# Kernel optimization log

Measured on AMD Instinct MI355X. Metric: run time of the kernel, lower is better.

The kernel has to match this reference:

```python
import jax, jax.numpy as jnp
import numpy as np
from jax import lax

H = 50; W = 50; C = 512; A = 9; P = 3; K = 2048; NC = 20
DIN = C * P * P  # 4608, flattened ROI-pooled feature


def _conv(x, w, b):
    # x [N,H,W,Cin], w [kh,kw,Cin,Cout]
    return lax.conv_general_dilated(x, w, (1, 1), 'SAME',
                                    dimension_numbers=('NHWC', 'HWIO', 'NHWC')) + b


def _roi_align(feat, boxes):
    # feat [H,W,C]; boxes [K,4] = (x1,x2,y1,y2) in feature-map coords -> [K,P,P,C]
    Hf, Wf, _ = feat.shape
    t = (jnp.arange(P, dtype=feat.dtype) + 0.5) / P
    xs = boxes[:, 0:1] + (boxes[:, 1:2] - boxes[:, 0:1]) * t  # [K,P]
    ys = boxes[:, 2:3] + (boxes[:, 3:4] - boxes[:, 2:3]) * t  # [K,P]
    x0f = jnp.floor(xs); y0f = jnp.floor(ys)
    fx = (xs - x0f)[:, None, :, None]  # [K,1,P,1]
    fy = (ys - y0f)[:, :, None, None]  # [K,P,1,1]
    x0 = jnp.clip(x0f.astype(jnp.int32), 0, Wf - 1); x1i = jnp.clip(x0 + 1, 0, Wf - 1)
    y0 = jnp.clip(y0f.astype(jnp.int32), 0, Hf - 1); y1i = jnp.clip(y0 + 1, 0, Hf - 1)

    def g(yi, xi):  # [K,P],[K,P] -> [K,P,P,C]
        return feat[yi[:, :, None], xi[:, None, :]]

    return (g(y0, x0) * (1 - fy) * (1 - fx) + g(y0, x1i) * (1 - fy) * fx
            + g(y1i, x0) * fy * (1 - fx) + g(y1i, x1i) * fy * fx)


def setup_inputs() -> dict:
    key = jax.random.key(0)
    ks = jax.random.split(key, 16)

    def w(k, shape, fan_in):
        return jax.random.normal(k, shape, jnp.float32) / np.float32(np.sqrt(fan_in))

    return {
        'features': jax.random.normal(ks[0], (1, H, W, C), jnp.float32),
        'labels': jax.random.randint(ks[1], (NC,), 0, 2, dtype=jnp.int32),
        'rpn_w': w(ks[2], (2, 2, C, C), 4 * C), 'rpn_b': jnp.zeros((C,), jnp.float32),
        'cls_w': w(ks[3], (1, 1, C, A), C), 'cls_b': jnp.zeros((A,), jnp.float32),
        'reg_w': w(ks[4], (1, 1, C, 4 * A), C), 'reg_b': jnp.zeros((4 * A,), jnp.float32),
        'fc6_w': w(ks[5], (DIN, 9216), DIN), 'fc6_b': jnp.zeros((9216,), jnp.float32),
        'fc7_w': w(ks[6], (9216, 4096), 9216), 'fc7_b': jnp.zeros((4096,), jnp.float32),
        'fc8c_w': w(ks[7], (4096, NC), 4096), 'fc8c_b': jnp.zeros((NC,), jnp.float32),
        'fc8d_w': w(ks[8], (4096, NC), 4096), 'fc8d_b': jnp.zeros((NC,), jnp.float32),
    }


def reference(features, labels, rpn_w, rpn_b, cls_w, cls_b, reg_w, reg_b,
              fc6_w, fc6_b, fc7_w, fc7_b, fc8c_w, fc8c_b, fc8d_w, fc8d_b):
    # RPN head
    x = jax.nn.relu(_conv(features, rpn_w, rpn_b))
    obj = jax.nn.sigmoid(_conv(x, cls_w, cls_b))  # [1,H,W,A] objectness
    reg = _conv(x, reg_w, reg_b)
    # Objectness filtering: fixed-size top-K replaces dynamic threshold filter
    _, idx = lax.top_k(obj.reshape(-1), K)
    raw = reg.reshape(-1, 4)[idx]                 # [K,4]
    s = jax.nn.sigmoid(raw)
    Wd = jnp.float32(W); Hd = jnp.float32(H)
    x1 = s[:, 0] * (Wd - 2.0); x2 = x1 + 1.0 + s[:, 1] * (Wd - 1.0 - x1)
    y1 = s[:, 2] * (Hd - 2.0); y2 = y1 + 1.0 + s[:, 3] * (Hd - 1.0 - y1)
    # original slices feature map with integer coords -> non-differentiable
    boxes = lax.stop_gradient(jnp.stack([x1, x2, y1, y2], axis=1))  # [K,4]
    # Per-ROI pooling (vectorized ROI-align)
    pooled = _roi_align(features[0], boxes).reshape(K, -1)  # [K,DIN]
    # FC trunk + two-stream WSDDN head
    h = jax.nn.relu(pooled @ fc6_w + fc6_b)
    h = jax.nn.relu(h @ fc7_w + fc7_b)
    c = jax.nn.softmax(h @ fc8c_w + fc8c_b, axis=0)  # softmax over regions
    d = jax.nn.softmax(h @ fc8d_w + fc8d_b, axis=1)  # softmax over classes
    scores = c * d                                   # [K,NC]
    output = jnp.clip(jnp.sum(scores, axis=0), 0.0, 1.0)  # [NC]
    return output, scores, boxes
```

## Files before the change

### kernel.cpp

```cpp
#include <hip/hip_runtime.h>
#include <math.h>


#define HN 50
#define WN 50
#define CN 512
#define AN 9
#define KTOP 2048
#define NCL 20
#define NOBJ 22500

typedef unsigned short ushort_t;
typedef __attribute__((ext_vector_type(8))) short short8;
typedef __attribute__((ext_vector_type(4))) float floatx4;

__device__ __forceinline__ ushort_t bf16_rne(float f) {
    unsigned int u = __float_as_uint(f);
    unsigned int r = (u + 0x7FFFu + ((u >> 16) & 1u)) >> 16;
    return (ushort_t)r;
}

__device__ __forceinline__ void gl_lds16(const void* g, void* l) {
    __builtin_amdgcn_global_load_lds(
        (const __attribute__((address_space(1))) unsigned int*)g,
        (__attribute__((address_space(3))) unsigned int*)l, 16, 0, 0);
}

__launch_bounds__(256)
__global__ void conv_chain_kernel(const float* __restrict__ feat,
                                  const float* __restrict__ rpnw,
                                  const float* __restrict__ rpnb,
                                  float* __restrict__ x32)
{
    __shared__ float xs[16 * 512];
    const int tid = threadIdx.x;
    const int hwBase = blockIdx.x * 4;
    const int co0 = tid * 2;

    for (int t = tid; t < 16 * 128; t += 256) {
        int slot = t >> 7, q = t & 127;
        int hwL = slot >> 2, tap = slot & 3;
        int hw = hwBase + hwL;
        int h = hw / WN, w = hw % WN;
        int hy = h + (tap >> 1), wx = w + (tap & 1);
        float4 v = make_float4(0.f, 0.f, 0.f, 0.f);
        if (hy < HN && wx < WN)
            v = *(const float4*)&feat[(size_t)(hy * WN + wx) * CN + q * 4];
        *(float4*)&xs[slot * 512 + q * 4] = v;
    }
    __syncthreads();

    float accx[4][4];
    float accy[4][4];
#pragma unroll
    for (int i = 0; i < 4; i++)
#pragma unroll
        for (int t = 0; t < 4; t++) { accx[i][t] = 0.f; accy[i][t] = 0.f; }

    const float* wbase = rpnw + co0;

    for (int cq = 0; cq < CN; cq += 4) {
        float4 xv[4][4];
#pragma unroll
        for (int i = 0; i < 4; i++)
#pragma unroll
            for (int t = 0; t < 4; t++)
                xv[i][t] = *(const float4*)&xs[(i * 4 + t) * 512 + cq];

#pragma unroll
        for (int cc = 0; cc < 4; cc++) {
            float2 wv[4];
#pragma unroll
            for (int t = 0; t < 4; t++)
                wv[t] = *(const float2*)&wbase[(size_t)(t * CN + cq + cc) * CN];
#pragma unroll
            for (int i = 0; i < 4; i++)
#pragma unroll
                for (int t = 0; t < 4; t++) {
                    float xvv = cc == 0 ? xv[i][t].x
                              : cc == 1 ? xv[i][t].y
                              : cc == 2 ? xv[i][t].z : xv[i][t].w;
                    accx[i][t] = fmaf(xvv, wv[t].x, accx[i][t]);
                    accy[i][t] = fmaf(xvv, wv[t].y, accy[i][t]);
                }
        }
    }

    float b0 = rpnb[co0], b1 = rpnb[co0 + 1];
#pragma unroll
    for (int i = 0; i < 4; i++) {
        float v0 = ((accx[i][0] + accx[i][1]) + accx[i][2]) + accx[i][3];
        float v1 = ((accy[i][0] + accy[i][1]) + accy[i][2]) + accy[i][3];
        v0 = v0 + b0; v1 = v1 + b1;
        v0 = v0 > 0.f ? v0 : 0.f;
        v1 = v1 > 0.f ? v1 : 0.f;
        float2 o = make_float2(v0, v1);
        *(float2*)&x32[(size_t)(hwBase + i) * CN + co0] = o;
    }
}

__launch_bounds__(256)
__global__ void obj_chain_kernel(const float* __restrict__ x32,
                                 const float* __restrict__ clsw,
                                 const float* __restrict__ clsb,
                                 float* __restrict__ key)
{
    int i = blockIdx.x * 256 + threadIdx.x;
    if (i >= NOBJ) return;
    int hw = i / AN, a = i % AN;
    const float* xr = x32 + (size_t)hw * CN;
    float acc = 0.f;
    for (int c = 0; c < CN; c++) acc = fmaf(xr[c], clsw[c * AN + a], acc);
    float l32 = acc + clsb[a];
    float s32 = (float)(1.0 / (1.0 + exp(-(double)l32)));
    key[i] = s32;
}

__launch_bounds__(256)
__global__ void topk_count_kernel(const float* __restrict__ key, int* __restrict__ cnt)
{
    __shared__ float ch[2048];
    int tid = threadIdx.x;
    int j0 = blockIdx.y * 2048;
    for (int t = tid; t < 2048; t += 256) {
        int jg = j0 + t;
        ch[t] = (jg < NOBJ) ? key[jg] : -1.0f;
    }
    int i = blockIdx.x * 256 + tid;
    float vi = (i < NOBJ) ? key[i] : 2.0f;
    __syncthreads();
    int c = 0;
    for (int t = 0; t < 2048; t++) {
        float vj = ch[t];
        int jg = j0 + t;
        c += (vj > vi || (vj == vi && jg < i)) ? 1 : 0;
    }
    if (i < NOBJ && c) atomicAdd(&cnt[i], c);
}

__launch_bounds__(256)
__global__ void topk_scatter_kernel(const int* __restrict__ cnt, int* __restrict__ sorted)
{
    int i = blockIdx.x * 256 + threadIdx.x;
    if (i < NOBJ) {
        int r = cnt[i];
        if (r < KTOP) sorted[r] = i;
    }
}

__launch_bounds__(256)
__global__ void boxes_kernel(const int* __restrict__ sorted,
                             const float* __restrict__ x32,
                             const float* __restrict__ regw,
                             const float* __restrict__ regb,
                             double* __restrict__ boxd,
                             float* __restrict__ outBoxes)
{
    int k = blockIdx.x * 256 + threadIdx.x;
    if (k >= KTOP) return;
    int i = sorted[k];
    int hw = i / AN, a = i % AN;
    const float* xr = x32 + (size_t)hw * CN;
    float r0 = 0.f, r1 = 0.f, r2 = 0.f, r3 = 0.f;
    for (int c = 0; c < CN; c++) {
        float xv = xr[c];
        const float* wr = regw + (size_t)c * (4 * AN) + 4 * a;
        r0 = fmaf(xv, wr[0], r0);
        r1 = fmaf(xv, wr[1], r1);
        r2 = fmaf(xv, wr[2], r2);
        r3 = fmaf(xv, wr[3], r3);
    }
    r0 = r0 + regb[4 * a + 0];
    r1 = r1 + regb[4 * a + 1];
    r2 = r2 + regb[4 * a + 2];
    r3 = r3 + regb[4 * a + 3];
    double s0 = 1.0 / (1.0 + exp(-(double)r0));
    double s1 = 1.0 / (1.0 + exp(-(double)r1));
    double s2 = 1.0 / (1.0 + exp(-(double)r2));
    double s3 = 1.0 / (1.0 + exp(-(double)r3));
    double x1 = s0 * (double)(WN - 2);
    double x2 = x1 + 1.0 + s1 * ((double)(WN - 1) - x1);
    double y1 = s2 * (double)(HN - 2);
    double y2 = y1 + 1.0 + s3 * ((double)(HN - 1) - y1);
    boxd[4 * k + 0] = x1; boxd[4 * k + 1] = x2;
    boxd[4 * k + 2] = y1; boxd[4 * k + 3] = y2;
    outBoxes[4 * k + 0] = (float)x1; outBoxes[4 * k + 1] = (float)x2;
    outBoxes[4 * k + 2] = (float)y1; outBoxes[4 * k + 3] = (float)y2;
}

__launch_bounds__(256)
__global__ void roi_kernel(const float* __restrict__ feat,
                           const double* __restrict__ boxd,
                           ushort_t* __restrict__ pooled)
{
    int k = blockIdx.x;
    int tid = threadIdx.x;
    double x1 = boxd[4 * k + 0], x2 = boxd[4 * k + 1];
    double y1 = boxd[4 * k + 2], y2 = boxd[4 * k + 3];
    int ix0[3], ix1[3], iy0[3], iy1[3];
    double fx[3], fy[3];
#pragma unroll
    for (int p = 0; p < 3; p++) {
        double t = ((double)p + 0.5) / 3.0;
        double xsv = x1 + (x2 - x1) * t;
        double x0f = floor(xsv);
        fx[p] = xsv - x0f;
        int xi = (int)x0f;
        xi = xi < 0 ? 0 : (xi > WN - 1 ? WN - 1 : xi);
        ix0[p] = xi;
        ix1[p] = (xi + 1 > WN - 1) ? WN - 1 : xi + 1;
        double ysv = y1 + (y2 - y1) * t;
        double y0f = floor(ysv);
        fy[p] = ysv - y0f;
        int yi = (int)y0f;
        yi = yi < 0 ? 0 : (yi > HN - 1 ? HN - 1 : yi);
        iy0[p] = yi;
        iy1[p] = (yi + 1 > HN - 1) ? HN - 1 : yi + 1;
    }
#pragma unroll
    for (int pp = 0; pp < 9; pp++) {
        int py = pp / 3, px = pp % 3;
        double w00 = (1.0 - fy[py]) * (1.0 - fx[px]);
        double w01 = (1.0 - fy[py]) * fx[px];
        double w10 = fy[py] * (1.0 - fx[px]);
        double w11 = fy[py] * fx[px];
        const float* f00 = feat + (size_t)(iy0[py] * WN + ix0[px]) * CN;
        const float* f01 = feat + (size_t)(iy0[py] * WN + ix1[px]) * CN;
        const float* f10 = feat + (size_t)(iy1[py] * WN + ix0[px]) * CN;
        const float* f11 = feat + (size_t)(iy1[py] * WN + ix1[px]) * CN;
        ushort_t* dst = pooled + ((size_t)k * 9 + pp) * CN;
        for (int c = tid; c < CN; c += 256) {
            double v = w00 * (double)f00[c] + w01 * (double)f01[c]
                     + w10 * (double)f10[c] + w11 * (double)f11[c];
            dst[c] = bf16_rne((float)v);
        }
    }
}

__launch_bounds__(256)
__global__ void transpose_cvt_kernel(const float* __restrict__ W,
                                     ushort_t* __restrict__ Wt,
                                     int K, int N, int n0)
{
    __shared__ float tile[64][65];
    const int tid = threadIdx.x;
    const int k0 = blockIdx.x * 64;
    const int nb = blockIdx.y * 64;
#pragma unroll
    for (int q = 0; q < 4; q++) {
        int r = (tid >> 4) + q * 16;
        int c = (tid & 15) * 4;
        float4 v = *(const float4*)&W[(size_t)(k0 + r) * N + n0 + nb + c];
        tile[r][c + 0] = v.x; tile[r][c + 1] = v.y;
        tile[r][c + 2] = v.z; tile[r][c + 3] = v.w;
    }
    __syncthreads();
#pragma unroll
    for (int q = 0; q < 4; q++) {
        int rn = (tid >> 4) + q * 16;
        int ck = (tid & 15) * 4;
        ushort4 o;
        o.x = bf16_rne(tile[ck + 0][rn]);
        o.y = bf16_rne(tile[ck + 1][rn]);
        o.z = bf16_rne(tile[ck + 2][rn]);
        o.w = bf16_rne(tile[ck + 3][rn]);
        *(ushort4*)&Wt[(size_t)(nb + rn) * K + k0 + ck] = o;
    }
}

__launch_bounds__(256)
__global__ void pack_w8_kernel(const float* __restrict__ cw,
                               const float* __restrict__ dw,
                               ushort_t* __restrict__ Wt8)
{
    int idx = blockIdx.x * 256 + threadIdx.x;
    int n = idx >> 12, k = idx & 4095;
    float v = 0.f;
    if (n < NCL) v = cw[(size_t)k * NCL + n];
    else if (n < 2 * NCL) v = dw[(size_t)k * NCL + (n - NCL)];
    Wt8[(size_t)n * 4096 + k] = bf16_rne(v);
}

__launch_bounds__(128)
__global__ void pack_b8_kernel(const float* __restrict__ cb,
                               const float* __restrict__ db,
                               float* __restrict__ b8)
{
    int n = threadIdx.x;
    float v = 0.f;
    if (n < NCL) v = cb[n];
    else if (n < 2 * NCL) v = db[n - NCL];
    b8[n] = v;
}

template <bool OUT_BF16, bool RELU>
__launch_bounds__(256)
__global__ void gemm_bt_kernel(const ushort_t* __restrict__ A,
                               const ushort_t* __restrict__ Bt,
                               const float* __restrict__ bias,
                               void* __restrict__ Cv,
                               int Nc, int K)
{
    __shared__ ushort_t As[128 * 32];
    __shared__ ushort_t Bs[128 * 32];
    const int tid = threadIdx.x;
    const int w = tid >> 6, l = tid & 63;
    const int mBase = blockIdx.y * 128, nBase = blockIdx.x * 128;
    const int mW = (w >> 1) * 64, nW = (w & 1) * 64;

    floatx4 acc[4][4];
#pragma unroll
    for (int i = 0; i < 4; i++)
#pragma unroll
        for (int j = 0; j < 4; j++) acc[i][j] = (floatx4){0.f, 0.f, 0.f, 0.f};

    const int r0 = tid >> 2;
    const int ce = (tid & 3) * 8;

    for (int kb = 0; kb < K; kb += 32) {
        __syncthreads();
        gl_lds16(&A[(size_t)(mBase + r0) * K + kb + ce], &As[tid * 8]);
        gl_lds16(&A[(size_t)(mBase + r0 + 64) * K + kb + ce], &As[2048 + tid * 8]);
        gl_lds16(&Bt[(size_t)(nBase + r0) * K + kb + ce], &Bs[tid * 8]);
        gl_lds16(&Bt[(size_t)(nBase + r0 + 64) * K + kb + ce], &Bs[2048 + tid * 8]);
        __syncthreads();

        short8 aF[4], bF[4];
#pragma unroll
        for (int i = 0; i < 4; i++)
            aF[i] = *(const short8*)&As[(mW + i * 16 + (l & 15)) * 32 + (l >> 4) * 8];
#pragma unroll
        for (int j = 0; j < 4; j++)
            bF[j] = *(const short8*)&Bs[(nW + j * 16 + (l & 15)) * 32 + (l >> 4) * 8];
#pragma unroll
        for (int i = 0; i < 4; i++)
#pragma unroll
            for (int j = 0; j < 4; j++)
                acc[i][j] = __builtin_amdgcn_mfma_f32_16x16x32_bf16(aF[i], bF[j], acc[i][j], 0, 0, 0);
    }

#pragma unroll
    for (int i = 0; i < 4; i++) {
        int rowT = mBase + mW + i * 16 + (l >> 4) * 4;
#pragma unroll
        for (int j = 0; j < 4; j++) {
            int col = nBase + nW + j * 16 + (l & 15);
            float bv = bias[col];
#pragma unroll
            for (int r = 0; r < 4; r++) {
                float v = acc[i][j][r] + bv;
                if (RELU) v = v > 0.f ? v : 0.f;
                size_t idx = (size_t)(rowT + r) * Nc + col;
                if (OUT_BF16) ((ushort_t*)Cv)[idx] = bf16_rne(v);
                else ((float*)Cv)[idx] = v;
            }
        }
    }
}

__launch_bounds__(256)
__global__ void colstats_kernel(const float* __restrict__ logits,
                                double* __restrict__ cmax, double* __restrict__ csum)
{
    __shared__ double red[4];
    int j = blockIdx.x, tid = threadIdx.x;
    double m = -1.0e300;
    for (int i = tid; i < KTOP; i += 256) m = fmax(m, (double)logits[(size_t)i * 128 + j]);
    for (int off = 32; off > 0; off >>= 1) m = fmax(m, __shfl_down(m, off, 64));
    if ((tid & 63) == 0) red[tid >> 6] = m;
    __syncthreads();
    double mm = fmax(fmax(red[0], red[1]), fmax(red[2], red[3]));
    __syncthreads();
    double s = 0.0;
    for (int i = tid; i < KTOP; i += 256) s += exp((double)logits[(size_t)i * 128 + j] - mm);
    for (int off = 32; off > 0; off >>= 1) s += __shfl_down(s, off, 64);
    if ((tid & 63) == 0) red[tid >> 6] = s;
    __syncthreads();
    if (tid == 0) { cmax[j] = mm; csum[j] = red[0] + red[1] + red[2] + red[3]; }
}

__launch_bounds__(256)
__global__ void scores_kernel(const float* __restrict__ logits,
                              const double* __restrict__ cmax, const double* __restrict__ csum,
                              double* __restrict__ scd, float* __restrict__ outScores)
{
    int i = blockIdx.x * 256 + threadIdx.x;
    if (i >= KTOP) return;
    const float* lr = logits + (size_t)i * 128;
    double rm = -1.0e300;
#pragma unroll
    for (int j = 0; j < NCL; j++) rm = fmax(rm, (double)lr[NCL + j]);
    double rs = 0.0;
#pragma unroll
    for (int j = 0; j < NCL; j++) rs += exp((double)lr[NCL + j] - rm);
#pragma unroll
    for (int j = 0; j < NCL; j++) {
        double cc = exp((double)lr[j] - cmax[j]) / csum[j];
        double dd = exp((double)lr[NCL + j] - rm) / rs;
        double sc = cc * dd;
        scd[(size_t)i * NCL + j] = sc;
        outScores[(size_t)i * NCL + j] = (float)sc;
    }
}

__launch_bounds__(256)
__global__ void colsum_kernel(const double* __restrict__ scd, float* __restrict__ out)
{
    __shared__ double red[4];
    int j = blockIdx.x, tid = threadIdx.x;
    double s = 0.0;
    for (int i = tid; i < KTOP; i += 256) s += scd[(size_t)i * NCL + j];
    for (int off = 32; off > 0; off >>= 1) s += __shfl_down(s, off, 64);
    if ((tid & 63) == 0) red[tid >> 6] = s;
    __syncthreads();
    if (tid == 0) {
        double t = red[0] + red[1] + red[2] + red[3];
        t = t < 0.0 ? 0.0 : (t > 1.0 ? 1.0 : t);
        out[j] = (float)t;
    }
}

extern "C" void kernel_launch(void* const* d_in, const int* in_sizes, int n_in,
                              void* d_out, int out_size, void* d_ws, size_t ws_size,
                              hipStream_t stream)
{
    const float* features = (const float*)d_in[0];
    const float* rpn_w  = (const float*)d_in[2];
    const float* rpn_b  = (const float*)d_in[3];
    const float* cls_w  = (const float*)d_in[4];
    const float* cls_b  = (const float*)d_in[5];
    const float* reg_w  = (const float*)d_in[6];
    const float* reg_b  = (const float*)d_in[7];
    const float* fc6_w  = (const float*)d_in[8];
    const float* fc6_b  = (const float*)d_in[9];
    const float* fc7_w  = (const float*)d_in[10];
    const float* fc7_b  = (const float*)d_in[11];
    const float* fc8c_w = (const float*)d_in[12];
    const float* fc8c_b = (const float*)d_in[13];
    const float* fc8d_w = (const float*)d_in[14];
    const float* fc8d_b = (const float*)d_in[15];

    float* out = (float*)d_out;
    char* ws = (char*)d_ws;

    const size_t OFF_H6   = 0;
    const size_t OFF_WT   = 37748736;
    const size_t OFF_ABF  = 80216064;
    const size_t OFF_H7   = 80216064;
    const size_t OFF_X32  = 0;
    const size_t OFF_KEY  = 5120000;
    const size_t OFF_CNT  = 5210112;
    const size_t OFF_SORT = 5300224;
    const size_t OFF_BOXD = 5308416;
    const size_t OFF_LOGIT = OFF_WT + 37748736;
    const size_t OFF_W8T   = OFF_LOGIT + 1048576;
    const size_t OFF_B8    = OFF_W8T + 1048576;
    const size_t OFF_SCD   = OFF_B8 + 512;
    const size_t OFF_CMAX  = OFF_SCD + 327680;
    const size_t OFF_CSUM  = OFF_CMAX + 512;

    float*    x32    = (float*)(ws + OFF_X32);
    float*    key    = (float*)(ws + OFF_KEY);
    int*      cnt    = (int*)(ws + OFF_CNT);
    int*      sorted = (int*)(ws + OFF_SORT);
    double*   boxd   = (double*)(ws + OFF_BOXD);
    ushort_t* Abf    = (ushort_t*)(ws + OFF_ABF);
    ushort_t* Wt     = (ushort_t*)(ws + OFF_WT);
    ushort_t* h6bf   = (ushort_t*)(ws + OFF_H6);
    ushort_t* h7bf   = (ushort_t*)(ws + OFF_H7);
    float*    logits = (float*)(ws + OFF_LOGIT);
    ushort_t* Wt8    = (ushort_t*)(ws + OFF_W8T);
    float*    b8     = (float*)(ws + OFF_B8);
    double*   scd    = (double*)(ws + OFF_SCD);
    double*   cmax   = (double*)(ws + OFF_CMAX);
    double*   csum   = (double*)(ws + OFF_CSUM);

    float* outScores = out + NCL;
    float* outBoxes  = out + NCL + KTOP * NCL;

    conv_chain_kernel<<<dim3(625), 256, 0, stream>>>(features, rpn_w, rpn_b, x32);
    obj_chain_kernel<<<dim3(88), 256, 0, stream>>>(x32, cls_w, cls_b, key);
    hipMemsetAsync(cnt, 0, NOBJ * sizeof(int), stream);
    topk_count_kernel<<<dim3(88, 11), 256, 0, stream>>>(key, cnt);
    topk_scatter_kernel<<<dim3(88), 256, 0, stream>>>(cnt, sorted);
    boxes_kernel<<<dim3(8), 256, 0, stream>>>(sorted, x32, reg_w, reg_b, boxd, outBoxes);

    roi_kernel<<<dim3(KTOP), 256, 0, stream>>>(features, boxd, Abf);

    transpose_cvt_kernel<<<dim3(72, 72), 256, 0, stream>>>(fc6_w, Wt, 4608, 9216, 0);
    gemm_bt_kernel<true, true><<<dim3(36, 16), 256, 0, stream>>>(Abf, Wt, fc6_b + 0,
                                                                 (void*)(h6bf + 0), 9216, 4608);
    transpose_cvt_kernel<<<dim3(72, 72), 256, 0, stream>>>(fc6_w, Wt, 4608, 9216, 4608);
    gemm_bt_kernel<true, true><<<dim3(36, 16), 256, 0, stream>>>(Abf, Wt, fc6_b + 4608,
                                                                 (void*)(h6bf + 4608), 9216, 4608);

    transpose_cvt_kernel<<<dim3(144, 32), 256, 0, stream>>>(fc7_w, Wt, 9216, 4096, 0);
    gemm_bt_kernel<true, true><<<dim3(16, 16), 256, 0, stream>>>(h6bf, Wt, fc7_b + 0,
                                                                 (void*)(h7bf + 0), 4096, 9216);
    transpose_cvt_kernel<<<dim3(144, 32), 256, 0, stream>>>(fc7_w, Wt, 9216, 4096, 2048);
    gemm_bt_kernel<true, true><<<dim3(16, 16), 256, 0, stream>>>(h6bf, Wt, fc7_b + 2048,
                                                                 (void*)(h7bf + 2048), 4096, 9216);

    pack_w8_kernel<<<dim3(2048), 256, 0, stream>>>(fc8c_w, fc8d_w, Wt8);
    pack_b8_kernel<<<dim3(1), 128, 0, stream>>>(fc8c_b, fc8d_b, b8);
    gemm_bt_kernel<false, false><<<dim3(1, 16), 256, 0, stream>>>(h7bf, Wt8, b8,
                                                                  (void*)logits, 128, 4096);

    colstats_kernel<<<dim3(NCL), 256, 0, stream>>>(logits, cmax, csum);
    scores_kernel<<<dim3(8), 256, 0, stream>>>(logits, cmax, csum, scd, outScores);
    colsum_kernel<<<dim3(NCL), 256, 0, stream>>>(scd, out);
}
```

Baseline: 1.557 ms.

## Triple-buffer GEMM LDS loads, swizzle blocks across XCDs, split-K the fc8 GEMM

```diff
diff --git a/kernel.cpp b/kernel.cpp
--- a/kernel.cpp
+++ b/kernel.cpp
@@ -59,20 +59,25 @@
 
     const float* wbase = rpnw + co0;
 
-    for (int cq = 0; cq < CN; cq += 4) {
+    float2 wA[4][4], wB[4][4];
+
+    auto loadw = [&](float2 (&wd)[4][4], int cqv) {
+#pragma unroll
+        for (int cc = 0; cc < 4; cc++)
+#pragma unroll
+            for (int t = 0; t < 4; t++)
+                wd[cc][t] = *(const float2*)&wbase[(size_t)(t * CN + cqv + cc) * CN];
+    };
+
+    auto dofma = [&](const float2 (&wd)[4][4], int cqv) {
         float4 xv[4][4];
 #pragma unroll
         for (int i = 0; i < 4; i++)
 #pragma unroll
             for (int t = 0; t < 4; t++)
-                xv[i][t] = *(const float4*)&xs[(i * 4 + t) * 512 + cq];
-
-#pragma unroll
-        for (int cc = 0; cc < 4; cc++) {
-            float2 wv[4];
-#pragma unroll
-            for (int t = 0; t < 4; t++)
-                wv[t] = *(const float2*)&wbase[(size_t)(t * CN + cq + cc) * CN];
+                xv[i][t] = *(const float4*)&xs[(i * 4 + t) * 512 + cqv];
+#pragma unroll
+        for (int cc = 0; cc < 4; cc++)
 #pragma unroll
             for (int i = 0; i < 4; i++)
 #pragma unroll
@@ -80,11 +85,21 @@
                     float xvv = cc == 0 ? xv[i][t].x
                               : cc == 1 ? xv[i][t].y
                               : cc == 2 ? xv[i][t].z : xv[i][t].w;
-                    accx[i][t] = fmaf(xvv, wv[t].x, accx[i][t]);
-                    accy[i][t] = fmaf(xvv, wv[t].y, accy[i][t]);
+                    accx[i][t] = fmaf(xvv, wd[cc][t].x, accx[i][t]);
+                    accy[i][t] = fmaf(xvv, wd[cc][t].y, accy[i][t]);
                 }
-        }
-    }
+    };
+
+    loadw(wA, 0);
+    for (int cq = 0; cq < CN - 8; cq += 8) {
+        loadw(wB, cq + 4);
+        dofma(wA, cq);
+        loadw(wA, cq + 8);
+        dofma(wB, cq + 4);
+    }
+    loadw(wB, CN - 4);
+    dofma(wA, CN - 8);
+    dofma(wB, CN - 4);
 
     float b0 = rpnb[co0], b1 = rpnb[co0 + 1];
 #pragma unroll
@@ -293,51 +308,77 @@
     b8[n] = v;
 }
 
-template <bool OUT_BF16, bool RELU>
+#define GEMM_STAGE(buf, kb)                                                                 \
+    gl_lds16(&A[(size_t)(mBase + (tid & 127)) * Krow + (kb) + (tid >> 7) * 8],              \
+             &As[buf][tid * 8]);                                                            \
+    gl_lds16(&A[(size_t)(mBase + (tid & 127)) * Krow + (kb) + ((tid >> 7) + 2) * 8],        \
+             &As[buf][(256 + tid) * 8]);                                                    \
+    gl_lds16(&Bt[(size_t)(nBase + (tid & 127)) * Krow + (kb) + (tid >> 7) * 8],             \
+             &Bs[buf][tid * 8]);                                                            \
+    gl_lds16(&Bt[(size_t)(nBase + (tid & 127)) * Krow + (kb) + ((tid >> 7) + 2) * 8],       \
+             &Bs[buf][(256 + tid) * 8]);
+
+template <bool OUT_BF16, bool RELU, bool SPLITK>
 __launch_bounds__(256)
 __global__ void gemm_bt_kernel(const ushort_t* __restrict__ A,
                                const ushort_t* __restrict__ Bt,
                                const float* __restrict__ bias,
                                void* __restrict__ Cv,
-                               int Nc, int K)
-{
-    __shared__ ushort_t As[128 * 32];
-    __shared__ ushort_t Bs[128 * 32];
+                               int Nc, int Krow, int kLen)
+{
+    __shared__ ushort_t As[3][128 * 32];
+    __shared__ ushort_t Bs[3][128 * 32];
     const int tid = threadIdx.x;
     const int w = tid >> 6, l = tid & 63;
-    const int mBase = blockIdx.y * 128, nBase = blockIdx.x * 128;
+
+    const int nwg = gridDim.x * gridDim.y;
+    const int hwid = blockIdx.y * gridDim.x + blockIdx.x;
+    const int q = nwg >> 3, r = nwg & 7;
+    const int xcd = hwid & 7, i0 = hwid >> 3;
+    const int swz = (xcd < r ? xcd * (q + 1) : r * (q + 1) + (xcd - r) * q) + i0;
+    const int nBase = (swz / gridDim.y) * 128;
+    const int mBase = (swz % gridDim.y) * 128;
     const int mW = (w >> 1) * 64, nW = (w & 1) * 64;
 
+    const int kb0 = SPLITK ? blockIdx.z * kLen : 0;
+    const int T = kLen / 32;
+
     floatx4 acc[4][4];
 #pragma unroll
     for (int i = 0; i < 4; i++)
 #pragma unroll
         for (int j = 0; j < 4; j++) acc[i][j] = (floatx4){0.f, 0.f, 0.f, 0.f};
 
-    const int r0 = tid >> 2;
-    const int ce = (tid & 3) * 8;
-
-    for (int kb = 0; kb < K; kb += 32) {
-        __syncthreads();
-        gl_lds16(&A[(size_t)(mBase + r0) * K + kb + ce], &As[tid * 8]);
-        gl_lds16(&A[(size_t)(mBase + r0 + 64) * K + kb + ce], &As[2048 + tid * 8]);
-        gl_lds16(&Bt[(size_t)(nBase + r0) * K + kb + ce], &Bs[tid * 8]);
-        gl_lds16(&Bt[(size_t)(nBase + r0 + 64) * K + kb + ce], &Bs[2048 + tid * 8]);
-        __syncthreads();
+    GEMM_STAGE(0, kb0);
+    GEMM_STAGE(1, kb0 + 32);
+
+    int cur = 0, nxt2 = 2;
+    for (int it = 0; it < T; ++it) {
+        if (it + 1 < T) asm volatile("s_waitcnt vmcnt(4)" ::: "memory");
+        else            asm volatile("s_waitcnt vmcnt(0)" ::: "memory");
+        __builtin_amdgcn_s_barrier();
+        __builtin_amdgcn_sched_barrier(0);
+        if (it + 2 < T) { GEMM_STAGE(nxt2, kb0 + (it + 2) * 32); }
 
         short8 aF[4], bF[4];
 #pragma unroll
         for (int i = 0; i < 4; i++)
-            aF[i] = *(const short8*)&As[(mW + i * 16 + (l & 15)) * 32 + (l >> 4) * 8];
+            aF[i] = *(const short8*)&As[cur][((l >> 4) * 128 + mW + i * 16 + (l & 15)) * 8];
 #pragma unroll
         for (int j = 0; j < 4; j++)
-            bF[j] = *(const short8*)&Bs[(nW + j * 16 + (l & 15)) * 32 + (l >> 4) * 8];
+            bF[j] = *(const short8*)&Bs[cur][((l >> 4) * 128 + nW + j * 16 + (l & 15)) * 8];
 #pragma unroll
         for (int i = 0; i < 4; i++)
 #pragma unroll
             for (int j = 0; j < 4; j++)
                 acc[i][j] = __builtin_amdgcn_mfma_f32_16x16x32_bf16(aF[i], bF[j], acc[i][j], 0, 0, 0);
-    }
+
+        cur = (cur == 2) ? 0 : cur + 1;
+        nxt2 = (nxt2 == 2) ? 0 : nxt2 + 1;
+    }
+
+    float* Cp = (float*)Cv;
+    if (SPLITK) Cp += (size_t)blockIdx.z * (size_t)gridDim.y * 128 * Nc;
 
 #pragma unroll
     for (int i = 0; i < 4; i++) {
@@ -345,17 +386,30 @@
 #pragma unroll
         for (int j = 0; j < 4; j++) {
             int col = nBase + nW + j * 16 + (l & 15);
-            float bv = bias[col];
-#pragma unroll
-            for (int r = 0; r < 4; r++) {
-                float v = acc[i][j][r] + bv;
+            float bv = SPLITK ? 0.f : bias[col];
+#pragma unroll
+            for (int r2 = 0; r2 < 4; r2++) {
+                float v = acc[i][j][r2] + bv;
                 if (RELU) v = v > 0.f ? v : 0.f;
-                size_t idx = (size_t)(rowT + r) * Nc + col;
+                size_t idx = (size_t)(rowT + r2) * Nc + col;
                 if (OUT_BF16) ((ushort_t*)Cv)[idx] = bf16_rne(v);
-                else ((float*)Cv)[idx] = v;
+                else Cp[idx] = v;
             }
         }
     }
+}
+
+__launch_bounds__(256)
+__global__ void reduce8_kernel(const float* __restrict__ P,
+                               const float* __restrict__ b8,
+                               float* __restrict__ logits)
+{
+    int idx = blockIdx.x * 256 + threadIdx.x;
+    int j = idx & 127;
+    float s = 0.f;
+#pragma unroll
+    for (int c = 0; c < 8; c++) s += P[(size_t)c * KTOP * 128 + idx];
+    logits[idx] = s + b8[j];
 }
 
 __launch_bounds__(256)
@@ -452,6 +506,7 @@
     const size_t OFF_CNT  = 5210112;
     const size_t OFF_SORT = 5300224;
     const size_t OFF_BOXD = 5308416;
+    const size_t OFF_P8   = OFF_WT;
     const size_t OFF_LOGIT = OFF_WT + 37748736;
     const size_t OFF_W8T   = OFF_LOGIT + 1048576;
     const size_t OFF_B8    = OFF_W8T + 1048576;
@@ -468,6 +523,7 @@
     ushort_t* Wt     = (ushort_t*)(ws + OFF_WT);
     ushort_t* h6bf   = (ushort_t*)(ws + OFF_H6);
     ushort_t* h7bf   = (ushort_t*)(ws + OFF_H7);
+    float*    P8     = (float*)(ws + OFF_P8);
     float*    logits = (float*)(ws + OFF_LOGIT);
     ushort_t* Wt8    = (ushort_t*)(ws + OFF_W8T);
     float*    b8     = (float*)(ws + OFF_B8);
@@ -488,23 +544,24 @@
     roi_kernel<<<dim3(KTOP), 256, 0, stream>>>(features, boxd, Abf);
 
     transpose_cvt_kernel<<<dim3(72, 72), 256, 0, stream>>>(fc6_w, Wt, 4608, 9216, 0);
-    gemm_bt_kernel<true, true><<<dim3(36, 16), 256, 0, stream>>>(Abf, Wt, fc6_b + 0,
-                                                                 (void*)(h6bf + 0), 9216, 4608);
+    gemm_bt_kernel<true, true, false><<<dim3(36, 16), 256, 0, stream>>>(
+        Abf, Wt, fc6_b + 0, (void*)(h6bf + 0), 9216, 4608, 4608);
     transpose_cvt_kernel<<<dim3(72, 72), 256, 0, stream>>>(fc6_w, Wt, 4608, 9216, 4608);
-    gemm_bt_kernel<true, true><<<dim3(36, 16), 256, 0, stream>>>(Abf, Wt, fc6_b + 4608,
-                                                                 (void*)(h6bf + 4608), 9216, 4608);
+    gemm_bt_kernel<true, true, false><<<dim3(36, 16), 256, 0, stream>>>(
+        Abf, Wt, fc6_b + 4608, (void*)(h6bf + 4608), 9216, 4608, 4608);
 
     transpose_cvt_kernel<<<dim3(144, 32), 256, 0, stream>>>(fc7_w, Wt, 9216, 4096, 0);
-    gemm_bt_kernel<true, true><<<dim3(16, 16), 256, 0, stream>>>(h6bf, Wt, fc7_b + 0,
-                                                                 (void*)(h7bf + 0), 4096, 9216);
+    gemm_bt_kernel<true, true, false><<<dim3(16, 16), 256, 0, stream>>>(
+        h6bf, Wt, fc7_b + 0, (void*)(h7bf + 0), 4096, 9216, 9216);
     transpose_cvt_kernel<<<dim3(144, 32), 256, 0, stream>>>(fc7_w, Wt, 9216, 4096, 2048);
-    gemm_bt_kernel<true, true><<<dim3(16, 16), 256, 0, stream>>>(h6bf, Wt, fc7_b + 2048,
-                                                                 (void*)(h7bf + 2048), 4096, 9216);
+    gemm_bt_kernel<true, true, false><<<dim3(16, 16), 256, 0, stream>>>(
+        h6bf, Wt, fc7_b + 2048, (void*)(h7bf + 2048), 4096, 9216, 9216);
 
     pack_w8_kernel<<<dim3(2048), 256, 0, stream>>>(fc8c_w, fc8d_w, Wt8);
     pack_b8_kernel<<<dim3(1), 128, 0, stream>>>(fc8c_b, fc8d_b, b8);
-    gemm_bt_kernel<false, false><<<dim3(1, 16), 256, 0, stream>>>(h7bf, Wt8, b8,
-                                                                  (void*)logits, 128, 4096);
+    gemm_bt_kernel<false, false, true><<<dim3(1, 16, 8), 256, 0, stream>>>(
+        h7bf, Wt8, b8, (void*)P8, 128, 4096, 512);
+    reduce8_kernel<<<dim3(1024), 256, 0, stream>>>(P8, b8, logits);
 
     colstats_kernel<<<dim3(NCL), 256, 0, stream>>>(logits, cmax, csum);
     scores_kernel<<<dim3(8), 256, 0, stream>>>(logits, cmax, csum, scd, outScores);
```

Measured after the change: 1.797 ms. +15.4%, slower.
